# Kernel optimization log

Hardware: AMD Instinct MI355X
Metric: run time of the kernel (lower is better)

The kernel has to match this reference:

```python
import jax, jax.numpy as jnp
import numpy as np

DIM = 512
INNER = 512          # heads * dim_head = 8 * 64
SCALE = 64 ** -0.5   # dim_head ** -0.5 (module uses this even though attention dim is INNER)
EPS = 1e-5


def _ln(x, g, b):
    m = jnp.mean(x, axis=-1, keepdims=True)
    v = jnp.var(x, axis=-1, keepdims=True)
    return (x - m) * jax.lax.rsqrt(v + EPS) * g + b


def setup_inputs() -> dict:
    key = jax.random.key(0)
    ks = jax.random.split(key, 5)
    B, T, C = 2, 32, 1024
    scaled = lambda k, sh, fan: jax.random.normal(k, sh, jnp.float32) * (fan ** -0.5)
    return {
        "x": jax.random.normal(ks[0], (B, T, C, DIM), jnp.float32),
        "gamma_t": jnp.ones((DIM,), jnp.float32),
        "beta_t": jnp.zeros((DIM,), jnp.float32),
        "w_qkv_t": scaled(ks[1], (DIM, 3 * INNER), DIM),
        "w_out_t": scaled(ks[2], (INNER, DIM), INNER),
        "b_out_t": jnp.zeros((DIM,), jnp.float32),
        "gamma_s": jnp.ones((DIM,), jnp.float32),
        "beta_s": jnp.zeros((DIM,), jnp.float32),
        "w_qkv_s": scaled(ks[3], (DIM, 3 * INNER), DIM),
        "w_out_s": scaled(ks[4], (INNER, DIM), INNER),
        "b_out_s": jnp.zeros((DIM,), jnp.float32),
    }


def reference(x, gamma_t, beta_t, w_qkv_t, w_out_t, b_out_t,
              gamma_s, beta_s, w_qkv_s, w_out_s, b_out_s):
    # ---- temporal attention (attend over t, per spatial token c) ----
    h = _ln(x, gamma_t, beta_t)                              # [b,t,c,D]
    q, k, v = jnp.split(h @ w_qkv_t, 3, axis=-1)             # each [b,t,c,I]
    q, k, v = (jnp.swapaxes(a, 1, 2) for a in (q, k, v))     # [b,c,t,I]
    attn = jax.nn.softmax(jnp.einsum('bcqd,bckd->bcqk', q, k) * SCALE, axis=-1)
    out = jnp.einsum('bcqk,bckd->bcqd', attn, v)             # [b,c,t,I]
    out = out @ w_out_t + b_out_t                            # [b,c,t,D]
    # ---- spatial attention (attend over c, per frame t) ----
    h = _ln(out, gamma_s, beta_s)                            # [b,c,t,D]
    q, k, v = jnp.split(h @ w_qkv_s, 3, axis=-1)             # each [b,c,t,I]
    q, k, v = (jnp.swapaxes(a, 1, 2) for a in (q, k, v))     # [b,t,c,I]
    attn = jax.nn.softmax(jnp.einsum('btqd,btkd->btqk', q, k) * SCALE, axis=-1)
    out = jnp.einsum('btqk,btkd->btqd', attn, v)             # [b,t,c,I]
    return out @ w_out_s + b_out_s                           # [b,t,c,D]
```

## Files before the change

kernel.cpp:

```cpp
#include <hip/hip_runtime.h>
#include <type_traits>

typedef unsigned short u16;
typedef _Float16 f16;
typedef f16 f16x8 __attribute__((ext_vector_type(8)));
typedef unsigned short u16x8 __attribute__((ext_vector_type(8)));
typedef unsigned short u16x4 __attribute__((ext_vector_type(4)));
typedef float f32x4 __attribute__((ext_vector_type(4)));

#define DEV __device__ __forceinline__

DEV u16 f2h(float f) { return __builtin_bit_cast(u16, (f16)f); }
DEV float h2f(u16 u) { return (float)__builtin_bit_cast(f16, u); }

DEV f32x4 mfma_f16(f16x8 a, f16x8 b, f32x4 c) {
  return __builtin_amdgcn_mfma_f32_16x16x32_f16(a, b, c, 0, 0, 0);
}
DEV f16x8 ldf16(const u16* p) { return *(const f16x8*)p; }

DEV void gl2lds16(const u16* g, u16* l) {
  __builtin_amdgcn_global_load_lds((const __attribute__((address_space(1))) void*)g,
                                   (__attribute__((address_space(3))) void*)l, 16, 0, 0);
}

DEV int swz(int row, int col) { return row * 64 + (col ^ ((row & 7) << 3)); }

DEV int xcd_remap(int d, int nwg) { return (d & 7) * (nwg >> 3) + (d >> 3); }

__global__ __launch_bounds__(256)
void wT_kernel(const float* __restrict__ W, u16* __restrict__ WT, int K, int N) {
  const int total = N * K;
  for (int i = blockIdx.x * 256 + threadIdx.x; i < total; i += gridDim.x * 256) {
    int n = i / K, k = i - n * K;
    WT[i] = f2h(W[(size_t)k * N + n]);
  }
}

__global__ __launch_bounds__(256)
void ln_kernel(const float* __restrict__ X, const float* __restrict__ G,
               const float* __restrict__ B, u16* __restrict__ H) {
  const int row = (blockIdx.x << 2) + (threadIdx.x >> 6);
  const int l = threadIdx.x & 63;
  const float* x = X + ((size_t)row << 9) + l * 8;
  float v[8];
  *(float4*)&v[0] = *(const float4*)(x);
  *(float4*)&v[4] = *(const float4*)(x + 4);
  float s = 0.f, s2 = 0.f;
#pragma unroll
  for (int e = 0; e < 8; ++e) { s += v[e]; s2 += v[e] * v[e]; }
#pragma unroll
  for (int o = 1; o < 64; o <<= 1) { s += __shfl_xor(s, o, 64); s2 += __shfl_xor(s2, o, 64); }
  const float mean = s * (1.f / 512.f);
  const float rs = rsqrtf(s2 * (1.f / 512.f) - mean * mean + 1e-5f);
  float g[8], bb[8];
  *(float4*)&g[0] = *(const float4*)(G + l * 8);
  *(float4*)&g[4] = *(const float4*)(G + l * 8 + 4);
  *(float4*)&bb[0] = *(const float4*)(B + l * 8);
  *(float4*)&bb[4] = *(const float4*)(B + l * 8 + 4);
  u16x8 o8;
#pragma unroll
  for (int e = 0; e < 8; ++e) o8[e] = f2h((v[e] - mean) * rs * g[e] + bb[e]);
  *(u16x8*)(H + ((size_t)row << 9) + l * 8) = o8;
}

__global__ __launch_bounds__(256)
void ln16_kernel(const u16* __restrict__ X, const float* __restrict__ G,
                 const float* __restrict__ B, u16* __restrict__ H) {
  const int row = (blockIdx.x << 2) + (threadIdx.x >> 6);
  const int l = threadIdx.x & 63;
  u16x8 raw = *(const u16x8*)(X + ((size_t)row << 9) + l * 8);
  float v[8];
#pragma unroll
  for (int e = 0; e < 8; ++e) v[e] = h2f(raw[e]);
  float s = 0.f, s2 = 0.f;
#pragma unroll
  for (int e = 0; e < 8; ++e) { s += v[e]; s2 += v[e] * v[e]; }
#pragma unroll
  for (int o = 1; o < 64; o <<= 1) { s += __shfl_xor(s, o, 64); s2 += __shfl_xor(s2, o, 64); }
  const float mean = s * (1.f / 512.f);
  const float rs = rsqrtf(s2 * (1.f / 512.f) - mean * mean + 1e-5f);
  float g[8], bb[8];
  *(float4*)&g[0] = *(const float4*)(G + l * 8);
  *(float4*)&g[4] = *(const float4*)(G + l * 8 + 4);
  *(float4*)&bb[0] = *(const float4*)(B + l * 8);
  *(float4*)&bb[4] = *(const float4*)(B + l * 8 + 4);
  u16x8 o8;
#pragma unroll
  for (int e = 0; e < 8; ++e) o8[e] = f2h((v[e] - mean) * rs * g[e] + bb[e]);
  *(u16x8*)(H + ((size_t)row << 9) + l * 8) = o8;
}

__global__ __launch_bounds__(256)
void gemm_qkv(const u16* __restrict__ A, const u16* __restrict__ Bt,
              u16* __restrict__ Cq, u16* __restrict__ Cv, int lda, int ldb, int K) {
  __shared__ u16 lds[2 * 128 * 64];
  u16* lsA = lds;
  u16* lsB = lds + 128 * 64;
  const int tid = threadIdx.x;
  const int w = tid >> 6, l = tid & 63;
  const int lr = l & 15, lg = l >> 4;
  const int wm = w >> 1, wn = w & 1;
  const int gx = gridDim.x;
  const int wk = xcd_remap(blockIdx.y * gx + blockIdx.x, gx * gridDim.y);
  const int Row0 = (wk / gx) * 128, Col0 = (wk % gx) * 128;
  const int gcol = ((l & 7) ^ (l >> 3)) * 8;

  f32x4 acc[4][4];
  const f32x4 zero = {0.f, 0.f, 0.f, 0.f};
#pragma unroll
  for (int m = 0; m < 4; ++m)
#pragma unroll
    for (int n = 0; n < 4; ++n) acc[m][n] = zero;

  for (int k0 = 0; k0 < K; k0 += 64) {
    __syncthreads();
#pragma unroll
    for (int i = 0; i < 4; ++i) {
      int row = w * 32 + i * 8 + (l >> 3);
      gl2lds16(A + (size_t)(Row0 + row) * lda + k0 + gcol, &lsA[w * 2048 + i * 512]);
      gl2lds16(Bt + (size_t)(Col0 + row) * ldb + k0 + gcol, &lsB[w * 2048 + i * 512]);
    }
    __syncthreads();
#pragma unroll
    for (int kk = 0; kk < 64; kk += 32) {
      f16x8 af[4], bfv[4];
#pragma unroll
      for (int m = 0; m < 4; ++m)
        af[m] = ldf16(&lsA[swz(wm * 64 + m * 16 + lr, kk + 8 * lg)]);
#pragma unroll
      for (int n = 0; n < 4; ++n)
        bfv[n] = ldf16(&lsB[swz(wn * 64 + n * 16 + lr, kk + 8 * lg)]);
#pragma unroll
      for (int m = 0; m < 4; ++m)
#pragma unroll
        for (int n = 0; n < 4; ++n) acc[m][n] = mfma_f16(af[m], bfv[n], acc[m][n]);
    }
  }

  const bool isV = (Col0 >= 1024);
#pragma unroll
  for (int p = 0; p < 2; ++p) {
    __syncthreads();
    if (wm == p) {
#pragma unroll
      for (int m = 0; m < 4; ++m)
#pragma unroll
        for (int n = 0; n < 4; ++n) {
          int col = wn * 64 + n * 16 + lr;
#pragma unroll
          for (int r = 0; r < 4; ++r)
            lds[(m * 16 + lg * 4 + r) * 136 + col] = f2h(acc[m][n][r]);
        }
    }
    __syncthreads();
#pragma unroll
    for (int it = 0; it < 4; ++it) {
      int cid = it * 256 + tid;
      int rl = cid >> 4, cc = (cid & 15) * 8;
      u16x8 vv = *(u16x8*)&lds[rl * 136 + cc];
      int gr = Row0 + p * 64 + rl;
      int gc = Col0 + cc;
      if (!isV)
        *(u16x8*)&Cq[(size_t)gr * 1024 + gc] = vv;
      else
        *(u16x8*)&Cv[(size_t)gr * 512 + gc - 1024] = vv;
    }
  }
}

template <bool OUT16, bool REMAP>
__global__ __launch_bounds__(256)
void gemm_bt(const u16* __restrict__ A, const u16* __restrict__ Bt,
             void* __restrict__ Cp, const float* __restrict__ bias,
             int lda, int ldb, int ldc, int K,
             long long sA, long long sB, long long sC, float scale) {
  __shared__ u16 lds[2 * 128 * 64];
  u16* lsA = lds;
  u16* lsB = lds + 128 * 64;
  const int tid = threadIdx.x;
  const int w = tid >> 6, l = tid & 63;
  const int lr = l & 15, lg = l >> 4;
  const int wm = w >> 1, wn = w & 1;
  int Row0, Col0;
  if constexpr (REMAP) {
    const int gx = gridDim.x;
    const int wk = xcd_remap(blockIdx.y * gx + blockIdx.x, gx * gridDim.y);
    Row0 = (wk / gx) * 128; Col0 = (wk % gx) * 128;
  } else {
    Row0 = blockIdx.y * 128; Col0 = blockIdx.x * 128;
  }
  const int bz = blockIdx.z;
  const int gcol = ((l & 7) ^ (l >> 3)) * 8;

  const u16* Ab = A + (size_t)bz * sA;
  const u16* Bb = Bt + (size_t)bz * sB;

  f32x4 acc[4][4];
  const f32x4 zero = {0.f, 0.f, 0.f, 0.f};
#pragma unroll
  for (int m = 0; m < 4; ++m)
#pragma unroll
    for (int n = 0; n < 4; ++n) acc[m][n] = zero;

  for (int k0 = 0; k0 < K; k0 += 64) {
    __syncthreads();
#pragma unroll
    for (int i = 0; i < 4; ++i) {
      int row = w * 32 + i * 8 + (l >> 3);
      gl2lds16(Ab + (size_t)(Row0 + row) * lda + k0 + gcol, &lsA[w * 2048 + i * 512]);
      gl2lds16(Bb + (size_t)(Col0 + row) * ldb + k0 + gcol, &lsB[w * 2048 + i * 512]);
    }
    __syncthreads();
#pragma unroll
    for (int kk = 0; kk < 64; kk += 32) {
      f16x8 af[4], bfv[4];
#pragma unroll
      for (int m = 0; m < 4; ++m)
        af[m] = ldf16(&lsA[swz(wm * 64 + m * 16 + lr, kk + 8 * lg)]);
#pragma unroll
      for (int n = 0; n < 4; ++n)
        bfv[n] = ldf16(&lsB[swz(wn * 64 + n * 16 + lr, kk + 8 * lg)]);
#pragma unroll
      for (int m = 0; m < 4; ++m)
#pragma unroll
        for (int n = 0; n < 4; ++n) acc[m][n] = mfma_f16(af[m], bfv[n], acc[m][n]);
    }
  }

  if constexpr (OUT16) {
    u16* Cb = (u16*)Cp + (size_t)bz * sC;
#pragma unroll
    for (int p = 0; p < 2; ++p) {
      __syncthreads();
      if (wm == p) {
#pragma unroll
        for (int m = 0; m < 4; ++m)
#pragma unroll
          for (int n = 0; n < 4; ++n) {
            int col = wn * 64 + n * 16 + lr;
            float bv = bias ? bias[Col0 + col] : 0.f;
#pragma unroll
            for (int r = 0; r < 4; ++r)
              lds[(m * 16 + lg * 4 + r) * 136 + col] = f2h(acc[m][n][r] * scale + bv);
          }
      }
      __syncthreads();
#pragma unroll
      for (int it = 0; it < 4; ++it) {
        int cid = it * 256 + tid;
        int rl = cid >> 4, cc = (cid & 15) * 8;
        u16x8 vv = *(u16x8*)&lds[rl * 136 + cc];
        *(u16x8*)&Cb[(size_t)(Row0 + p * 64 + rl) * ldc + Col0 + cc] = vv;
      }
    }
  } else {
    float* Cb = (float*)Cp + (size_t)bz * sC;
#pragma unroll
    for (int m = 0; m < 4; ++m)
#pragma unroll
      for (int n = 0; n < 4; ++n) {
        int gc = Col0 + wn * 64 + n * 16 + lr;
        float bv = bias ? bias[gc] : 0.f;
#pragma unroll
        for (int r = 0; r < 4; ++r) {
          int gr = Row0 + wm * 64 + m * 16 + lg * 4 + r;
          Cb[(size_t)gr * ldc + gc] = acc[m][n][r] * scale + bv;
        }
      }
  }
}

__global__ __launch_bounds__(256)
void attn_t_kernel(const u16* __restrict__ QK, const u16* __restrict__ Vb,
                   u16* __restrict__ O) {
  __shared__ u16 qs[32 * 520];
  __shared__ u16 ks[32 * 520];
  __shared__ u16 vT[512 * 40];
  __shared__ float Sf[32 * 32];
  __shared__ u16 Pf[32 * 40];

  const int tid = threadIdx.x;
  const int bc = blockIdx.x;
  const int w = tid >> 6, l = tid & 63, lr = l & 15, lg = l >> 4;
  const int wr = w >> 1, wc = w & 1;
  const size_t base = (size_t)(bc >> 10) * 32768 + (bc & 1023);

#pragma unroll
  for (int i = 0; i < 8; ++i) {
    int t = w * 8 + i;
    const u16* rb = QK + (base + (size_t)t * 1024) * 1024;
    gl2lds16(rb + l * 8, &qs[t * 520]);
    gl2lds16(rb + 512 + l * 8, &ks[t * 520]);
  }
#pragma unroll
  for (int j = 0; j < 8; ++j) {
    int li = j * 2048 + tid * 8;
    int t = li >> 9, col = li & 511;
    u16x8 vv = *(const u16x8*)(Vb + (base + (size_t)t * 1024) * 512 + col);
#pragma unroll
    for (int e = 0; e < 8; ++e) vT[(col + e) * 40 + t] = vv[e];
  }
  __syncthreads();

  f32x4 sacc = {0.f, 0.f, 0.f, 0.f};
#pragma unroll
  for (int kk = 0; kk < 512; kk += 32)
    sacc = mfma_f16(ldf16(&qs[(wr * 16 + lr) * 520 + kk + 8 * lg]),
                    ldf16(&ks[(wc * 16 + lr) * 520 + kk + 8 * lg]), sacc);
#pragma unroll
  for (int r = 0; r < 4; ++r)
    Sf[(wr * 16 + lg * 4 + r) * 32 + wc * 16 + lr] = sacc[r] * 0.125f;
  __syncthreads();

  if (tid < 32) {
    float mx = -1e30f;
    for (int j = 0; j < 32; ++j) mx = fmaxf(mx, Sf[tid * 32 + j]);
    float s = 0.f;
    for (int j = 0; j < 32; ++j) s += __expf(Sf[tid * 32 + j] - mx);
    float inv = 1.f / s;
    for (int j = 0; j < 32; ++j) Pf[tid * 40 + j] = f2h(__expf(Sf[tid * 32 + j] - mx) * inv);
  }
  __syncthreads();

  {
    const int mr = w >> 1, nh = w & 1;
    f16x8 ap = ldf16(&Pf[(mr * 16 + lr) * 40 + 8 * lg]);
#pragma unroll
    for (int j = 0; j < 16; ++j) {
      int nc = (nh * 16 + j) * 16;
      f32x4 o = {0.f, 0.f, 0.f, 0.f};
      o = mfma_f16(ap, ldf16(&vT[(nc + lr) * 40 + 8 * lg]), o);
#pragma unroll
      for (int r = 0; r < 4; ++r)
        qs[(mr * 16 + lg * 4 + r) * 520 + nc + lr] = f2h(o[r]);
    }
  }
  __syncthreads();
#pragma unroll
  for (int it = 0; it < 8; ++it) {
    int cid = it * 256 + tid;
    int t = cid >> 6, col = (cid & 63) * 8;
    u16x8 vv = *(u16x8*)&qs[t * 520 + col];
    *(u16x8*)&O[(base + (size_t)t * 1024) * 512 + col] = vv;
  }
}

__global__ __launch_bounds__(256)
void softmax16_kernel(u16* __restrict__ S) {
  u16* p = S + ((size_t)blockIdx.x << 10);
  const int tid = threadIdx.x, w = tid >> 6, l = tid & 63;
  __shared__ float red[8];
  u16x4 raw = *(u16x4*)&p[tid << 2];
  float v0 = h2f(raw[0]), v1 = h2f(raw[1]), v2 = h2f(raw[2]), v3 = h2f(raw[3]);
  float m = fmaxf(fmaxf(v0, v1), fmaxf(v2, v3));
#pragma unroll
  for (int o = 1; o < 64; o <<= 1) m = fmaxf(m, __shfl_xor(m, o, 64));
  if (l == 0) red[w] = m;
  __syncthreads();
  m = fmaxf(fmaxf(red[0], red[1]), fmaxf(red[2], red[3]));
  v0 = __expf(v0 - m); v1 = __expf(v1 - m); v2 = __expf(v2 - m); v3 = __expf(v3 - m);
  float s = v0 + v1 + v2 + v3;
#pragma unroll
  for (int o = 1; o < 64; o <<= 1) s += __shfl_xor(s, o, 64);
  if (l == 0) red[4 + w] = s;
  __syncthreads();
  const float inv = 1.f / (red[4] + red[5] + red[6] + red[7]);
  u16x4 o4 = {f2h(v0 * inv), f2h(v1 * inv), f2h(v2 * inv), f2h(v3 * inv)};
  *(u16x4*)&p[tid << 2] = o4;
}

__global__ __launch_bounds__(256)
void transpose_v_kernel(const u16* __restrict__ Vb, u16* __restrict__ Vt) {
  __shared__ u16 tl[64][72];
  const int bt = blockIdx.z;
  const int c0 = blockIdx.x << 6, d0 = blockIdx.y << 6;
  const int tid = threadIdx.x;
#pragma unroll
  for (int pass = 0; pass < 2; ++pass) {
    int r = (pass << 5) + (tid >> 3), cc = (tid & 7) << 3;
    *(u16x8*)&tl[r][cc] = *(const u16x8*)(Vb + ((size_t)(bt * 1024 + c0 + r)) * 512 + d0 + cc);
  }
  __syncthreads();
#pragma unroll
  for (int pass = 0; pass < 2; ++pass) {
    int rd = (pass << 5) + (tid >> 3), cc = (tid & 7) << 3;
    u16x8 o;
#pragma unroll
    for (int e = 0; e < 8; ++e) o[e] = tl[cc + e][rd];
    *(u16x8*)(Vt + ((size_t)(bt * 512 + d0 + rd)) * 1024 + c0 + cc) = o;
  }
}

extern "C" void kernel_launch(void* const* d_in, const int* in_sizes, int n_in,
                              void* d_out, int out_size, void* d_ws, size_t ws_size,
                              hipStream_t stream) {
  (void)in_sizes; (void)n_in; (void)out_size; (void)ws_size;
  const float* x      = (const float*)d_in[0];
  const float* gam_t  = (const float*)d_in[1];
  const float* bet_t  = (const float*)d_in[2];
  const float* wqkv_t = (const float*)d_in[3];
  const float* wout_t = (const float*)d_in[4];
  const float* bout_t = (const float*)d_in[5];
  const float* gam_s  = (const float*)d_in[6];
  const float* bet_s  = (const float*)d_in[7];
  const float* wqkv_s = (const float*)d_in[8];
  const float* wout_s = (const float*)d_in[9];
  const float* bout_s = (const float*)d_in[10];
  float* out = (float*)d_out;

  char* ws = (char*)d_ws;
  size_t off = 0;
  auto alloc = [&](size_t bytes) -> char* {
    char* p = ws + off;
    off = (off + bytes + 255) & ~(size_t)255;
    return p;
  };
  u16* wqkvT_t = (u16*)alloc((size_t)1536 * 512 * 2);
  u16* woutT_t = (u16*)alloc((size_t)512 * 512 * 2);
  u16* wqkvT_s = (u16*)alloc((size_t)1536 * 512 * 2);
  u16* woutT_s = (u16*)alloc((size_t)512 * 512 * 2);
  u16* QK      = (u16*)alloc((size_t)65536 * 1024 * 2);
  u16* Vb      = (u16*)alloc((size_t)65536 * 512 * 2);
  u16* attnO   = (u16*)alloc((size_t)65536 * 512 * 2);
  u16* S       = (u16*)alloc((size_t)32 * 1024 * 1024 * 2);
  u16* vT      = (u16*)alloc((size_t)32 * 512 * 1024 * 2);
  u16* h       = S;
  u16* out1    = QK;

  const dim3 blk(256);

  wT_kernel<<<768, blk, 0, stream>>>(wqkv_t, wqkvT_t, 512, 1536);
  wT_kernel<<<256, blk, 0, stream>>>(wout_t, woutT_t, 512, 512);
  wT_kernel<<<768, blk, 0, stream>>>(wqkv_s, wqkvT_s, 512, 1536);
  wT_kernel<<<256, blk, 0, stream>>>(wout_s, woutT_s, 512, 512);

  ln_kernel<<<16384, blk, 0, stream>>>(x, gam_t, bet_t, h);
  gemm_qkv<<<dim3(12, 512, 1), blk, 0, stream>>>(h, wqkvT_t, QK, Vb, 512, 512, 512);
  attn_t_kernel<<<2048, blk, 0, stream>>>(QK, Vb, attnO);
  gemm_bt<true, true><<<dim3(4, 512, 1), blk, 0, stream>>>(
      attnO, woutT_t, out1, bout_t, 512, 512, 512, 512, 0, 0, 0, 1.f);

  ln16_kernel<<<16384, blk, 0, stream>>>(out1, gam_s, bet_s, h);
  gemm_qkv<<<dim3(12, 512, 1), blk, 0, stream>>>(h, wqkvT_s, QK, Vb, 512, 512, 512);

  for (int ch = 0; ch < 2; ++ch) {
    const u16* qkc = QK + (size_t)ch * 32 * 1024 * 1024;
    const u16* vbc = Vb + (size_t)ch * 32 * 1024 * 512;
    u16* attc = attnO + (size_t)ch * 32 * 1024 * 512;
    transpose_v_kernel<<<dim3(16, 8, 32), blk, 0, stream>>>(vbc, vT);
    gemm_bt<true, false><<<dim3(8, 8, 32), blk, 0, stream>>>(
        qkc, qkc + 512, S, nullptr, 1024, 1024, 1024, 512,
        1024LL * 1024, 1024LL * 1024, 1024LL * 1024, 0.125f);
    softmax16_kernel<<<32768, blk, 0, stream>>>(S);
    gemm_bt<true, false><<<dim3(4, 8, 32), blk, 0, stream>>>(
        S, vT, attc, nullptr, 1024, 1024, 512, 1024,
        1024LL * 1024, 512LL * 1024, 1024LL * 512, 1.f);
  }

  gemm_bt<false, true><<<dim3(4, 512, 1), blk, 0, stream>>>(
      attnO, woutT_s, out, bout_s, 512, 512, 512, 512, 0, 0, 0, 1.f);
}
```

Before: 954.9 us.

## Fuse weight transposes, stage fp32 GEMM stores, parallelize temporal softmax

Merges the four weight-transpose launches into one kernel. Precomputes per-row GEMM load pointers and advances them each k-step instead of recomputing addresses. Routes the fp32 GEMM epilogue through LDS so stores become coalesced float4 rows. In temporal attention it reorders the V transpose loads and spreads the 32-row softmax across all 256 threads with shuffles instead of 32 serial threads. It adds extra syncs in the epilogue.

```diff
diff --git a/kernel.cpp b/kernel.cpp
--- a/kernel.cpp
+++ b/kernel.cpp
@@ -28,11 +28,23 @@
 DEV int xcd_remap(int d, int nwg) { return (d & 7) * (nwg >> 3) + (d >> 3); }
 
 __global__ __launch_bounds__(256)
-void wT_kernel(const float* __restrict__ W, u16* __restrict__ WT, int K, int N) {
-  const int total = N * K;
-  for (int i = blockIdx.x * 256 + threadIdx.x; i < total; i += gridDim.x * 256) {
-    int n = i / K, k = i - n * K;
-    WT[i] = f2h(W[(size_t)k * N + n]);
+void wT_all_kernel(const float* __restrict__ Wq_t, const float* __restrict__ Wo_t,
+                   const float* __restrict__ Wq_s, const float* __restrict__ Wo_s,
+                   u16* __restrict__ Tq_t, u16* __restrict__ To_t,
+                   u16* __restrict__ Tq_s, u16* __restrict__ To_s) {
+  const int bid = blockIdx.x;
+  const float* W;
+  u16* T;
+  int N, base;
+  if (bid < 768)       { W = Wq_t; T = Tq_t; N = 1536; base = bid; }
+  else if (bid < 1024) { W = Wo_t; T = To_t; N = 512;  base = bid - 768; }
+  else if (bid < 1792) { W = Wq_s; T = Tq_s; N = 1536; base = bid - 1024; }
+  else                 { W = Wo_s; T = To_s; N = 512;  base = bid - 1792; }
+#pragma unroll
+  for (int j = 0; j < 4; ++j) {
+    int i = base * 1024 + j * 256 + threadIdx.x;
+    int n = i >> 9, k = i & 511;
+    T[i] = f2h(W[(size_t)k * N + n]);
   }
 }
 
@@ -105,6 +117,15 @@
   const int Row0 = (wk / gx) * 128, Col0 = (wk % gx) * 128;
   const int gcol = ((l & 7) ^ (l >> 3)) * 8;
 
+  const u16* pA[4];
+  const u16* pB[4];
+#pragma unroll
+  for (int i = 0; i < 4; ++i) {
+    int row = w * 32 + i * 8 + (l >> 3);
+    pA[i] = A + (size_t)(Row0 + row) * lda + gcol;
+    pB[i] = Bt + (size_t)(Col0 + row) * ldb + gcol;
+  }
+
   f32x4 acc[4][4];
   const f32x4 zero = {0.f, 0.f, 0.f, 0.f};
 #pragma unroll
@@ -116,9 +137,10 @@
     __syncthreads();
 #pragma unroll
     for (int i = 0; i < 4; ++i) {
-      int row = w * 32 + i * 8 + (l >> 3);
-      gl2lds16(A + (size_t)(Row0 + row) * lda + k0 + gcol, &lsA[w * 2048 + i * 512]);
-      gl2lds16(Bt + (size_t)(Col0 + row) * ldb + k0 + gcol, &lsB[w * 2048 + i * 512]);
+      gl2lds16(pA[i], &lsA[w * 2048 + i * 512]);
+      gl2lds16(pB[i], &lsB[w * 2048 + i * 512]);
+      pA[i] += 64;
+      pB[i] += 64;
     }
     __syncthreads();
 #pragma unroll
@@ -194,6 +216,14 @@
 
   const u16* Ab = A + (size_t)bz * sA;
   const u16* Bb = Bt + (size_t)bz * sB;
+  const u16* pA[4];
+  const u16* pB[4];
+#pragma unroll
+  for (int i = 0; i < 4; ++i) {
+    int row = w * 32 + i * 8 + (l >> 3);
+    pA[i] = Ab + (size_t)(Row0 + row) * lda + gcol;
+    pB[i] = Bb + (size_t)(Col0 + row) * ldb + gcol;
+  }
 
   f32x4 acc[4][4];
   const f32x4 zero = {0.f, 0.f, 0.f, 0.f};
@@ -206,9 +236,10 @@
     __syncthreads();
 #pragma unroll
     for (int i = 0; i < 4; ++i) {
-      int row = w * 32 + i * 8 + (l >> 3);
-      gl2lds16(Ab + (size_t)(Row0 + row) * lda + k0 + gcol, &lsA[w * 2048 + i * 512]);
-      gl2lds16(Bb + (size_t)(Col0 + row) * ldb + k0 + gcol, &lsB[w * 2048 + i * 512]);
+      gl2lds16(pA[i], &lsA[w * 2048 + i * 512]);
+      gl2lds16(pB[i], &lsB[w * 2048 + i * 512]);
+      pA[i] += 64;
+      pB[i] += 64;
     }
     __syncthreads();
 #pragma unroll
@@ -255,18 +286,34 @@
     }
   } else {
     float* Cb = (float*)Cp + (size_t)bz * sC;
-#pragma unroll
-    for (int m = 0; m < 4; ++m)
-#pragma unroll
-      for (int n = 0; n < 4; ++n) {
-        int gc = Col0 + wn * 64 + n * 16 + lr;
-        float bv = bias ? bias[gc] : 0.f;
-#pragma unroll
-        for (int r = 0; r < 4; ++r) {
-          int gr = Row0 + wm * 64 + m * 16 + lg * 4 + r;
-          Cb[(size_t)gr * ldc + gc] = acc[m][n][r] * scale + bv;
+    float* ldsF = (float*)lds;
+#pragma unroll
+    for (int q = 0; q < 4; ++q) {
+      __syncthreads();
+      if (wm == (q >> 1)) {
+        int mBase = (q & 1) * 2;
+#pragma unroll
+        for (int mi = 0; mi < 2; ++mi) {
+          int m = mBase + mi;
+#pragma unroll
+          for (int n = 0; n < 4; ++n) {
+            int col = wn * 64 + n * 16 + lr;
+            float bv = bias ? bias[Col0 + col] : 0.f;
+#pragma unroll
+            for (int r = 0; r < 4; ++r)
+              ldsF[(mi * 16 + lg * 4 + r) * 132 + col] = acc[m][n][r] * scale + bv;
+          }
         }
       }
+      __syncthreads();
+#pragma unroll
+      for (int it = 0; it < 4; ++it) {
+        int cid = it * 256 + tid;
+        int rw = cid >> 5, c4 = (cid & 31) * 4;
+        float4 v = *(float4*)&ldsF[rw * 132 + c4];
+        *(float4*)&Cb[(size_t)(Row0 + q * 32 + rw) * ldc + Col0 + c4] = v;
+      }
+    }
   }
 }
 
@@ -276,7 +323,7 @@
   __shared__ u16 qs[32 * 520];
   __shared__ u16 ks[32 * 520];
   __shared__ u16 vT[512 * 40];
-  __shared__ float Sf[32 * 32];
+  __shared__ float Sf[32 * 36];
   __shared__ u16 Pf[32 * 40];
 
   const int tid = threadIdx.x;
@@ -292,13 +339,17 @@
     gl2lds16(rb + l * 8, &qs[t * 520]);
     gl2lds16(rb + 512 + l * 8, &ks[t * 520]);
   }
-#pragma unroll
-  for (int j = 0; j < 8; ++j) {
-    int li = j * 2048 + tid * 8;
-    int t = li >> 9, col = li & 511;
-    u16x8 vv = *(const u16x8*)(Vb + (base + (size_t)t * 1024) * 512 + col);
-#pragma unroll
-    for (int e = 0; e < 8; ++e) vT[(col + e) * 40 + t] = vv[e];
+  {
+    const int t = tid & 31;
+    const int db0 = (tid >> 5) * 8;
+    const u16* vrow = Vb + (base + (size_t)t * 1024) * 512;
+#pragma unroll
+    for (int j = 0; j < 8; ++j) {
+      int db = db0 + j;
+      u16x8 vv = *(const u16x8*)(vrow + db * 8);
+#pragma unroll
+      for (int e = 0; e < 8; ++e) vT[(db * 8 + e) * 40 + t] = vv[e];
+    }
   }
   __syncthreads();
 
@@ -309,16 +360,23 @@
                     ldf16(&ks[(wc * 16 + lr) * 520 + kk + 8 * lg]), sacc);
 #pragma unroll
   for (int r = 0; r < 4; ++r)
-    Sf[(wr * 16 + lg * 4 + r) * 32 + wc * 16 + lr] = sacc[r] * 0.125f;
-  __syncthreads();
-
-  if (tid < 32) {
-    float mx = -1e30f;
-    for (int j = 0; j < 32; ++j) mx = fmaxf(mx, Sf[tid * 32 + j]);
-    float s = 0.f;
-    for (int j = 0; j < 32; ++j) s += __expf(Sf[tid * 32 + j] - mx);
-    float inv = 1.f / s;
-    for (int j = 0; j < 32; ++j) Pf[tid * 40 + j] = f2h(__expf(Sf[tid * 32 + j] - mx) * inv);
+    Sf[(wr * 16 + lg * 4 + r) * 36 + wc * 16 + lr] = sacc[r] * 0.125f;
+  __syncthreads();
+
+  {
+    const int row = tid >> 3, c0 = (tid & 7) * 4;
+    float4 sv = *(float4*)&Sf[row * 36 + c0];
+    float mx = fmaxf(fmaxf(sv.x, sv.y), fmaxf(sv.z, sv.w));
+#pragma unroll
+    for (int o = 1; o < 8; o <<= 1) mx = fmaxf(mx, __shfl_xor(mx, o, 64));
+    float e0 = __expf(sv.x - mx), e1 = __expf(sv.y - mx);
+    float e2 = __expf(sv.z - mx), e3 = __expf(sv.w - mx);
+    float sum = e0 + e1 + e2 + e3;
+#pragma unroll
+    for (int o = 1; o < 8; o <<= 1) sum += __shfl_xor(sum, o, 64);
+    float inv = 1.f / sum;
+    u16x4 p4 = {f2h(e0 * inv), f2h(e1 * inv), f2h(e2 * inv), f2h(e3 * inv)};
+    *(u16x4*)&Pf[row * 40 + c0] = p4;
   }
   __syncthreads();
 
@@ -429,10 +487,8 @@
 
   const dim3 blk(256);
 
-  wT_kernel<<<768, blk, 0, stream>>>(wqkv_t, wqkvT_t, 512, 1536);
-  wT_kernel<<<256, blk, 0, stream>>>(wout_t, woutT_t, 512, 512);
-  wT_kernel<<<768, blk, 0, stream>>>(wqkv_s, wqkvT_s, 512, 1536);
-  wT_kernel<<<256, blk, 0, stream>>>(wout_s, woutT_s, 512, 512);
+  wT_all_kernel<<<2048, blk, 0, stream>>>(wqkv_t, wout_t, wqkv_s, wout_s,
+                                          wqkvT_t, woutT_t, wqkvT_s, woutT_s);
 
   ln_kernel<<<16384, blk, 0, stream>>>(x, gam_t, bet_t, h);
   gemm_qkv<<<dim3(12, 512, 1), blk, 0, stream>>>(h, wqkvT_t, QK, Vb, 512, 512, 512);
```

Result: faster. 893.4 us (-6.4%).
